# Optimization experiments

Measured on AMD Instinct MI355X. Metric: run time of the kernel, lower is better.

## Reference

```python
import jax, jax.numpy as jnp
import numpy as np

EPS = 1e-6
P_GEN = -9.0          # generalized-mean exponent (soft-min over grid)
BETA = 0.2            # bounded-IoU smooth-L1 transition point
HM_WEIGHT = 1.0
WH_WEIGHT = 0.1


def setup_inputs() -> dict:
    key = jax.random.key(0)
    ks = jax.random.split(key, 8)
    S, B, K, H, W = 2, 16, 128, 128, 128
    hm = jax.random.normal(ks[0], (S, B, 1, H, W), dtype=jnp.float32)
    # wh maps / targets must be positive (widths/heights on the stride-4 grid)
    wh_map = jax.random.uniform(ks[1], (S, B, 2, H, W), dtype=jnp.float32) * 30.0 + 1.0
    reg_map = jax.random.uniform(ks[2], (S, B, 2, H, W), dtype=jnp.float32)
    reg_gt = jax.random.uniform(ks[3], (B, K, 2), dtype=jnp.float32)
    wh_gt = jax.random.uniform(ks[4], (B, K, 2), dtype=jnp.float32) * 30.0 + 1.0
    ind = jax.random.randint(ks[5], (B, K), 0, H * W, dtype=jnp.int32)
    ctr = jax.random.randint(ks[6], (B, K, 2), 0, min(H, W), dtype=jnp.int32)
    reg_mask = jax.random.randint(ks[7], (B, K), 0, 2, dtype=jnp.int32)
    return {"hm": hm, "wh_map": wh_map, "reg_map": reg_map,
            "reg_gt": reg_gt, "wh_gt": wh_gt,
            "ind": ind, "ctr": ctr, "reg_mask": reg_mask}


def _gather_feat(feat, ind):
    # feat: (S,B,C,H,W), ind: (B,K) flat indices into H*W -> (S,B,K,C)
    S, B, C, H, W = feat.shape
    f = feat.reshape(S, B, C, H * W).transpose(0, 1, 3, 2)   # (S,B,HW,C)
    return jnp.take_along_axis(f, ind[None, :, :, None], axis=2)


def _whd_one(p_map, pts, m, grid, max_dist):
    # Weighted Hausdorff distance for one sample.
    # p_map: (H,W) probs; pts: (K,2) [y,x] float; m: (K,) {0,1} float
    p = p_map.reshape(-1)                                    # (HW,)
    d = jnp.sqrt(((grid[:, None, :] - pts[None, :, :]) ** 2).sum(-1))  # (HW,K)
    n_est = p.sum()
    # term 1: invalid points excluded from the min (max_dist upper-bounds all d)
    dmin = jnp.where(m[None, :] > 0, d, max_dist).min(axis=1)
    term1 = (p * dmin).sum() / (n_est + EPS)
    # term 2: soft-min over grid via generalized mean with p=-9
    weighted = (1.0 - p)[:, None] * max_dist + p[:, None] * d  # (HW,K)
    minn = jnp.mean((weighted + EPS) ** P_GEN, axis=0) ** (1.0 / P_GEN)  # (K,)
    term2 = (minn * m).sum() / jnp.maximum(m.sum(), 1.0)
    return term1 + term2


def _bounded_iou(reg_g, wh_g, reg_p, wh_p, m):
    # reg_g/wh_g: (1,B,K,2) gt; reg_p/wh_p: (S,B,K,2) pred; m: (B,K)
    dx = reg_g[..., 0] - reg_p[..., 0]
    dy = reg_g[..., 1] - reg_p[..., 1]
    w_g, h_g = wh_g[..., 0], wh_g[..., 1]
    w_p, h_p = wh_p[..., 0], wh_p[..., 1]
    ldx = 1.0 - jnp.maximum((w_g - 2.0 * jnp.abs(dx)) / (w_g + 2.0 * jnp.abs(dx) + EPS), 0.0)
    ldy = 1.0 - jnp.maximum((h_g - 2.0 * jnp.abs(dy)) / (h_g + 2.0 * jnp.abs(dy) + EPS), 0.0)
    ldw = 1.0 - jnp.minimum(w_g / (w_p + EPS), w_p / (w_g + EPS))
    ldh = 1.0 - jnp.minimum(h_g / (h_p + EPS), h_p / (h_g + EPS))
    l = jnp.stack([ldx, ldy, ldw, ldh], -1)                  # (S,B,K,4)
    l = jnp.where(l < BETA, 0.5 * l * l / BETA, l - 0.5 * BETA)
    num = (l * m[None, :, :, None]).sum((-1, -2))            # (S,B)
    den = jnp.maximum(m.sum(-1), 1.0)[None, :] * 4.0
    return num / den


def _forward(hm, wh_map, reg_map, reg_gt, wh_gt, ind, ctr, reg_mask):
    S, B, _, H, W = hm.shape
    dt = hm.dtype
    hm_p = jnp.clip(jax.nn.sigmoid(hm), 1e-4, 1.0 - 1e-4)    # CenterNet _sigmoid
    WH = _gather_feat(wh_map, ind)                            # (S,B,K,2)
    REG = _gather_feat(reg_map, ind)                          # (S,B,K,2)
    m = reg_mask.astype(dt)                                   # (B,K)
    valid = (m.sum(-1) > 0).astype(dt)                        # (B,) -> skip empty samples

    ys, xs = jnp.meshgrid(jnp.arange(H), jnp.arange(W), indexing="ij")
    grid = jnp.stack([ys, xs], -1).reshape(-1, 2).astype(dt)  # (HW,2)
    max_dist = jnp.sqrt(jnp.asarray(H * H + W * W, dt))
    pts = ctr[..., ::-1].astype(dt)                           # (B,K,2) [y,x]

    whd_batch = jax.vmap(_whd_one, in_axes=(0, 0, 0, None, None))
    hm_terms = jax.vmap(lambda hms: whd_batch(hms, pts, m, grid, max_dist))(hm_p[:, :, 0])  # (S,B)
    hm_loss = (hm_terms * valid[None, :]).sum() / (B * S)

    iou_terms = _bounded_iou(reg_gt[None], wh_gt[None], REG, WH, m)  # (S,B)
    iou_loss = (iou_terms * valid[None, :]).sum() / (B * S)

    loss = HM_WEIGHT * hm_loss + WH_WEIGHT * iou_loss
    return loss, hm_loss, iou_loss


def reference(hm, wh_map, reg_map, reg_gt, wh_gt, ind, ctr, reg_mask):
    return _forward(hm, wh_map, reg_map, reg_gt, wh_gt, ind, ctr, reg_mask)
```

## Files before the change

### kernel.cpp

```cpp
#include <hip/hip_runtime.h>

#define SS 2
#define BB 16
#define KK 128
#define HH 128
#define WW 128
#define HWSZ (HH*WW)
#define EPSF 1e-6f
#define MAXD 181.01933598375618f
#define MAXD2 32768.0f
#define MAXD8 (181.01933598375618f * 0.125f)
#define ME8C ((181.01933598375618f + 1e-6f) * 0.125f)

typedef float v2f __attribute__((ext_vector_type(2)));

#define WSQ_OFF 524288
#define WS_NEEDED_BYTES ((size_t)(524288 + 16*128*4) * 4)

__device__ __forceinline__ float sigclip(float x) {
    float e = __expf(-x);
    float p = __builtin_amdgcn_rcpf(1.0f + e);
    return fminf(fmaxf(p, 1e-4f), 0.9999f);
}

__device__ __forceinline__ float smoothl1(float l) {
    return (l < 0.2f) ? (2.5f * l * l) : (l - 0.1f);
}


__global__ void __launch_bounds__(256, 6) kAB2(const float* __restrict__ hm,
                                               const int* __restrict__ ctr,
                                               const int* __restrict__ reg_mask,
                                               float* __restrict__ ws,
                                               float* __restrict__ out) {
    const int r = blockIdx.x;
    const int b = blockIdx.y;
    const int t = threadIdx.x;
    __shared__ __align__(16) float spp2[128][2];
    __shared__ float2 spts_raw[KK];
    __shared__ float2 spts_msk[KK];
    __shared__ float red0[KK], red1[KK];
    __shared__ float st2[128];
    __shared__ float sred[8];

    if (r == 0 && b == 0 && t < 3) out[t] = 0.0f;

    {
        int c = t >> 7, j = t & 127;
        spp2[j][c] = sigclip(hm[(size_t)(c * BB + b) * HWSZ + r * WW + j]);
    }
    if (t < KK) {
        int mk = reg_mask[b * KK + t];
        float py = (float)ctr[(b * KK + t) * 2 + 1];
        float px = (float)ctr[(b * KK + t) * 2 + 0];
        spts_raw[t] = make_float2(py, px);
        spts_msk[t] = mk ? make_float2(py, px) : make_float2(1e9f, 1e9f);
    }
    __syncthreads();

    const int k = t & 127;
    const int h = t >> 7;

    float acc0 = 0.f, acc1 = 0.f;
    {
        float2 pt = spts_raw[k];
        float dy = ((float)r - pt.x) * 0.125f;
        float dy2 = dy * dy;
        float dx = ((float)(h * 64) - pt.y) * 0.125f;
        const float4* sp4 = (const float4*)(&spp2[h * 64][0]);
        const v2f ME8V = {ME8C, ME8C};
        #pragma unroll 4
        for (int q = 0; q < 32; ++q) {
            float4 pq = sp4[q];
            float dA = __builtin_amdgcn_sqrtf(fmaf(dx, dx, dy2));
            float dxB = dx + 0.125f;
            float dB = __builtin_amdgcn_sqrtf(fmaf(dxB, dxB, dy2));
            float tA = dA - MAXD8;
            float tB = dB - MAXD8;
            v2f pA = {pq.x, pq.y};
            v2f pB = {pq.z, pq.w};
            v2f wA = pA * tA + ME8V;
            v2f wB = pB * tB + ME8V;
            v2f a2 = wA * wA, a4 = a2 * a2, a8 = a4 * a4, a9 = a8 * wA;
            v2f b2 = wB * wB, b4 = b2 * b2, b8 = b4 * b4, b9 = b8 * wB;
            v2f pr = a9 * b9;
            v2f sm = a9 + b9;
            acc0 = fmaf(sm.x, __builtin_amdgcn_rcpf(pr.x), acc0);
            acc1 = fmaf(sm.y, __builtin_amdgcn_rcpf(pr.y), acc1);
            dx += 0.25f;
        }
    }

    float mm;
    {
        int pix = t & 127;
        float fx = (float)pix, fyf = (float)r;
        float m0 = MAXD2, m1 = MAXD2, m2 = MAXD2, m3 = MAXD2;
        int kb = h * 64;
        #pragma unroll 4
        for (int kk = 0; kk < 64; kk += 4) {
            float2 q0 = spts_msk[kb + kk + 0];
            float2 q1 = spts_msk[kb + kk + 1];
            float2 q2 = spts_msk[kb + kk + 2];
            float2 q3 = spts_msk[kb + kk + 3];
            float e0 = fyf - q0.x, f0 = fx - q0.y;
            float e1 = fyf - q1.x, f1 = fx - q1.y;
            float e2 = fyf - q2.x, f2 = fx - q2.y;
            float e3 = fyf - q3.x, f3 = fx - q3.y;
            m0 = fminf(m0, fmaf(f0, f0, e0 * e0));
            m1 = fminf(m1, fmaf(f1, f1, e1 * e1));
            m2 = fminf(m2, fmaf(f2, f2, e2 * e2));
            m3 = fminf(m3, fmaf(f3, f3, e3 * e3));
        }
        mm = fminf(fminf(m0, m1), fminf(m2, m3));
    }

    if (t >= 128) { st2[k] = mm; red0[k] = acc0; red1[k] = acc1; }
    __syncthreads();

    if (t < 128) {
        float s0 = acc0 + red0[k];
        float s1 = acc1 + red1[k];
        size_t basep = ((size_t)(b * 128 + r) * 2) * 128;
        ws[basep + k] = s0;
        ws[basep + 128 + k] = s1;
        float dmin = __builtin_amdgcn_sqrtf(fminf(mm, st2[k]));
        float p0 = spp2[k][0], p1 = spp2[k][1];
        float t1a = p0 * dmin, t1b = p1 * dmin, nea = p0, neb = p1;
        #pragma unroll
        for (int off = 32; off > 0; off >>= 1) {
            t1a += __shfl_down(t1a, off, 64);
            t1b += __shfl_down(t1b, off, 64);
            nea += __shfl_down(nea, off, 64);
            neb += __shfl_down(neb, off, 64);
        }
        if ((t & 63) == 0) {
            int wv = t >> 6;
            sred[wv * 4 + 0] = t1a; sred[wv * 4 + 1] = t1b;
            sred[wv * 4 + 2] = nea; sred[wv * 4 + 3] = neb;
        }
    }
    __syncthreads();
    if (t == 0) {
        float4 v = make_float4(sred[0] + sred[4], sred[1] + sred[5],
                               sred[2] + sred[6], sred[3] + sred[7]);
        ((float4*)(ws + WSQ_OFF))[b * 128 + r] = v;
    }
}

__global__ void __launch_bounds__(256) kC2(const float* __restrict__ ws,
                                           const float* __restrict__ wh_map,
                                           const float* __restrict__ reg_map,
                                           const float* __restrict__ reg_gt,
                                           const float* __restrict__ wh_gt,
                                           const int* __restrict__ ind,
                                           const int* __restrict__ reg_mask,
                                           float* __restrict__ out) {
    const int b = blockIdx.x, s = blockIdx.y;
    const int t = threadIdx.x;
    const int k = t & 127;
    const int g = t >> 7;

    __shared__ float ssum[256];
    {
        float sum = 0.f;
        const float* base = ws + ((size_t)(b * 128 + g * 64) * 2 + s) * 128 + k;
        #pragma unroll 8
        for (int c = 0; c < 64; ++c) sum += base[(size_t)c * 256];
        ssum[t] = sum;
    }
    __syncthreads();
    if (t >= 128) return;

    float mk = (float)reg_mask[b * KK + k];
    float meanp = (ssum[k] + ssum[k + 128]) * (1.0f / 16384.0f);
    float c2 = (mk > 0.f) ? 8.0f * exp2f(log2f(meanp) * (-1.0f / 9.0f)) : 0.0f;

    float g1 = 0.f, g2 = 0.f;
    {
        float4 q = ((const float4*)(ws + WSQ_OFF))[b * 128 + k];
        g1 = s ? q.y : q.x;
        g2 = s ? q.w : q.z;
        #pragma unroll
        for (int off = 32; off > 0; off >>= 1) {
            g1 += __shfl_down(g1, off, 64);
            g2 += __shfl_down(g2, off, 64);
        }
    }
    __shared__ float st1[2], sne[2];
    if ((k & 63) == 0) { st1[k >> 6] = g1; sne[k >> 6] = g2; }

    int idx = ind[b * KK + k];
    size_t sb = (size_t)(s * BB + b);
    float rp0 = reg_map[(sb * 2 + 0) * HWSZ + idx];
    float rp1 = reg_map[(sb * 2 + 1) * HWSZ + idx];
    float wp0 = wh_map[(sb * 2 + 0) * HWSZ + idx];
    float wp1 = wh_map[(sb * 2 + 1) * HWSZ + idx];
    float rg0 = reg_gt[(b * KK + k) * 2 + 0];
    float rg1 = reg_gt[(b * KK + k) * 2 + 1];
    float wg0 = wh_gt[(b * KK + k) * 2 + 0];
    float wg1 = wh_gt[(b * KK + k) * 2 + 1];
    float adx = fabsf(rg0 - rp0), ady = fabsf(rg1 - rp1);
    float ldx = 1.0f - fmaxf((wg0 - 2.0f * adx) / (wg0 + 2.0f * adx + EPSF), 0.0f);
    float ldy = 1.0f - fmaxf((wg1 - 2.0f * ady) / (wg1 + 2.0f * ady + EPSF), 0.0f);
    float ldw = 1.0f - fminf(wg0 / (wp0 + EPSF), wp0 / (wg0 + EPSF));
    float ldh = 1.0f - fminf(wg1 / (wp1 + EPSF), wp1 / (wg1 + EPSF));
    float lsum = (smoothl1(ldx) + smoothl1(ldy) + smoothl1(ldw) + smoothl1(ldh)) * mk;

    #pragma unroll
    for (int off = 32; off > 0; off >>= 1) {
        c2   += __shfl_down(c2, off, 64);
        lsum += __shfl_down(lsum, off, 64);
        mk   += __shfl_down(mk, off, 64);
    }
    __shared__ float sred[6];
    int lane = k & 63, wv = k >> 6;
    if (lane == 0) { sred[wv * 3 + 0] = c2; sred[wv * 3 + 1] = lsum; sred[wv * 3 + 2] = mk; }
    __syncthreads();
    if (k == 0) {
        float C2 = sred[0] + sred[3];
        float LS = sred[1] + sred[4];
        float MS = sred[2] + sred[5];
        float t1n = st1[0] + st1[1];
        float nst = sne[0] + sne[1];
        float valid = (MS > 0.f) ? 1.f : 0.f;
        float den = fmaxf(MS, 1.f);
        float t1 = t1n / (nst + EPSF);
        float t2 = C2 / den;
        float hmterm  = (t1 + t2) * valid * (1.0f / 32.0f);
        float iouterm = (LS / (den * 4.0f)) * valid * (1.0f / 32.0f);
        atomicAdd(&out[1], hmterm);
        atomicAdd(&out[2], iouterm);
        atomicAdd(&out[0], hmterm + 0.1f * iouterm);
    }
}


__global__ void kzero(float* ws, float* out) {
    int i = blockIdx.x * 256 + threadIdx.x;
    if (i < 4160) ws[i] = 0.0f;
    if (i < 3) out[i] = 0.0f;
}

__global__ void __launch_bounds__(256) kAB(const float* __restrict__ hm,
                                           const int* __restrict__ ctr,
                                           const int* __restrict__ reg_mask,
                                           float* __restrict__ ws) {
    const int b = blockIdx.y;
    const int chunk = blockIdx.x;
    const int base = chunk * 256;
    const int tid = threadIdx.x;
    __shared__ float2 spp[256];
    __shared__ float2 spts_raw[KK];
    __shared__ float2 spts_msk[KK];
    __shared__ float red0[KK], red1[KK];

    float p0 = sigclip(hm[(size_t)(0 * BB + b) * HWSZ + base + tid]);
    float p1 = sigclip(hm[(size_t)(1 * BB + b) * HWSZ + base + tid]);
    spp[tid] = make_float2(p0, p1);
    if (tid < KK) {
        int mk = reg_mask[b * KK + tid];
        float py = (float)ctr[(b * KK + tid) * 2 + 1];
        float px = (float)ctr[(b * KK + tid) * 2 + 0];
        spts_raw[tid] = make_float2(py, px);
        spts_msk[tid] = mk ? make_float2(py, px) : make_float2(1e9f, 1e9f);
    }
    __syncthreads();

    const int k = tid & 127;
    const int half = tid >> 7;
    float2 pt = spts_raw[k];
    float fy1 = (float)(chunk * 2 + half);
    float dy2 = (fy1 - pt.x) * (fy1 - pt.x);
    float acc0 = 0.f, acc1 = 0.f;
    float dx = -pt.y;
    const float2* sp = &spp[half * 128];
    #pragma unroll 4
    for (int j = 0; j < 128; ++j) {
        float d = __builtin_amdgcn_sqrtf(fmaf(dx, dx, dy2));
        float t = d - MAXD;
        float2 p = sp[j];
        float w0 = fmaf(p.x, t, MAXD) + EPSF;
        float w1 = fmaf(p.y, t, MAXD) + EPSF;
        float a2 = w0 * w0, a4 = a2 * a2, a8 = a4 * a4;
        float b2 = w1 * w1, b4 = b2 * b2, b8 = b4 * b4;
        acc0 += __builtin_amdgcn_rcpf(a8 * w0);
        acc1 += __builtin_amdgcn_rcpf(b8 * w1);
        dx += 1.0f;
    }

    {
        float fy = (float)(chunk * 2 + (tid >> 7));
        float fx = (float)(tid & 127);
        float m0 = MAXD2, m1 = MAXD2, m2 = MAXD2, m3 = MAXD2;
        #pragma unroll 4
        for (int kk = 0; kk < KK; kk += 4) {
            float2 q0 = spts_msk[kk + 0];
            float2 q1 = spts_msk[kk + 1];
            float2 q2 = spts_msk[kk + 2];
            float2 q3 = spts_msk[kk + 3];
            float dy0 = fy - q0.x, dx0 = fx - q0.y;
            float dy1 = fy - q1.x, dx1 = fx - q1.y;
            float dy2_ = fy - q2.x, dx2 = fx - q2.y;
            float dy3 = fy - q3.x, dx3 = fx - q3.y;
            m0 = fminf(m0, fmaf(dx0, dx0, dy0 * dy0));
            m1 = fminf(m1, fmaf(dx1, dx1, dy1 * dy1));
            m2 = fminf(m2, fmaf(dx2, dx2, dy2_ * dy2_));
            m3 = fminf(m3, fmaf(dx3, dx3, dy3 * dy3));
        }
        float dmin = __builtin_amdgcn_sqrtf(fminf(fminf(m0, m1), fminf(m2, m3)));
        float t1a = p0 * dmin, t1b = p1 * dmin, nea = p0, neb = p1;
        #pragma unroll
        for (int off = 32; off > 0; off >>= 1) {
            t1a += __shfl_down(t1a, off, 64);
            t1b += __shfl_down(t1b, off, 64);
            nea += __shfl_down(nea, off, 64);
            neb += __shfl_down(neb, off, 64);
        }
        if ((tid & 63) == 0) {
            atomicAdd(&ws[4096 + 0 * BB + b], t1a);
            atomicAdd(&ws[4096 + 1 * BB + b], t1b);
            atomicAdd(&ws[4128 + 0 * BB + b], nea);
            atomicAdd(&ws[4128 + 1 * BB + b], neb);
        }
    }

    if (half) { red0[k] = acc0; red1[k] = acc1; }
    __syncthreads();
    if (!half) {
        atomicAdd(&ws[(0 * BB + b) * KK + k], acc0 + red0[k]);
        atomicAdd(&ws[(1 * BB + b) * KK + k], acc1 + red1[k]);
    }
}

__global__ void __launch_bounds__(128) kC(const float* __restrict__ ws,
                                          const float* __restrict__ wh_map,
                                          const float* __restrict__ reg_map,
                                          const float* __restrict__ reg_gt,
                                          const float* __restrict__ wh_gt,
                                          const int* __restrict__ ind,
                                          const int* __restrict__ reg_mask,
                                          float* __restrict__ out) {
    const int b = blockIdx.x, s = blockIdx.y, k = threadIdx.x;
    float mk = (float)reg_mask[b * KK + k];
    float sp = ws[(s * BB + b) * KK + k];
    float mean = sp * (1.0f / 16384.0f);
    float c2 = (mk > 0.f) ? exp2f(log2f(mean) * (-1.0f / 9.0f)) : 0.0f;

    int idx = ind[b * KK + k];
    size_t sb = (size_t)(s * BB + b);
    float rp0 = reg_map[(sb * 2 + 0) * HWSZ + idx];
    float rp1 = reg_map[(sb * 2 + 1) * HWSZ + idx];
    float wp0 = wh_map[(sb * 2 + 0) * HWSZ + idx];
    float wp1 = wh_map[(sb * 2 + 1) * HWSZ + idx];
    float rg0 = reg_gt[(b * KK + k) * 2 + 0];
    float rg1 = reg_gt[(b * KK + k) * 2 + 1];
    float wg0 = wh_gt[(b * KK + k) * 2 + 0];
    float wg1 = wh_gt[(b * KK + k) * 2 + 1];
    float adx = fabsf(rg0 - rp0), ady = fabsf(rg1 - rp1);
    float ldx = 1.0f - fmaxf((wg0 - 2.0f * adx) / (wg0 + 2.0f * adx + EPSF), 0.0f);
    float ldy = 1.0f - fmaxf((wg1 - 2.0f * ady) / (wg1 + 2.0f * ady + EPSF), 0.0f);
    float ldw = 1.0f - fminf(wg0 / (wp0 + EPSF), wp0 / (wg0 + EPSF));
    float ldh = 1.0f - fminf(wg1 / (wp1 + EPSF), wp1 / (wg1 + EPSF));
    float lsum = (smoothl1(ldx) + smoothl1(ldy) + smoothl1(ldw) + smoothl1(ldh)) * mk;

    #pragma unroll
    for (int off = 32; off > 0; off >>= 1) {
        c2   += __shfl_down(c2, off, 64);
        lsum += __shfl_down(lsum, off, 64);
        mk   += __shfl_down(mk, off, 64);
    }
    __shared__ float sred[6];
    int lane = k & 63, wv = k >> 6;
    if (lane == 0) { sred[wv * 3 + 0] = c2; sred[wv * 3 + 1] = lsum; sred[wv * 3 + 2] = mk; }
    __syncthreads();
    if (k == 0) {
        float C2 = sred[0] + sred[3];
        float LS = sred[1] + sred[4];
        float MS = sred[2] + sred[5];
        float valid = (MS > 0.f) ? 1.f : 0.f;
        float den = fmaxf(MS, 1.f);
        float t1 = ws[4096 + s * BB + b] / (ws[4128 + s * BB + b] + EPSF);
        float t2 = C2 / den;
        float hmterm  = (t1 + t2) * valid * (1.0f / 32.0f);
        float iouterm = (LS / (den * 4.0f)) * valid * (1.0f / 32.0f);
        atomicAdd(&out[1], hmterm);
        atomicAdd(&out[2], iouterm);
        atomicAdd(&out[0], hmterm + 0.1f * iouterm);
    }
}

extern "C" void kernel_launch(void* const* d_in, const int* in_sizes, int n_in,
                              void* d_out, int out_size, void* d_ws, size_t ws_size,
                              hipStream_t stream) {
    const float* hm       = (const float*)d_in[0];
    const float* wh_map   = (const float*)d_in[1];
    const float* reg_map  = (const float*)d_in[2];
    const float* reg_gt   = (const float*)d_in[3];
    const float* wh_gt    = (const float*)d_in[4];
    const int*   ind      = (const int*)d_in[5];
    const int*   ctr      = (const int*)d_in[6];
    const int*   reg_mask = (const int*)d_in[7];
    float* out = (float*)d_out;
    float* ws  = (float*)d_ws;

    if (ws_size >= WS_NEEDED_BYTES) {
        hipLaunchKernelGGL(kAB2, dim3(128, BB), dim3(256), 0, stream,
                           hm, ctr, reg_mask, ws, out);
        hipLaunchKernelGGL(kC2, dim3(BB, SS), dim3(256), 0, stream,
                           ws, wh_map, reg_map, reg_gt, wh_gt, ind, reg_mask, out);
    } else {
        hipLaunchKernelGGL(kzero, dim3(17), dim3(256), 0, stream, ws, out);
        hipLaunchKernelGGL(kAB, dim3(64, BB), dim3(256), 0, stream, hm, ctr, reg_mask, ws);
        hipLaunchKernelGGL(kC, dim3(BB, SS), dim3(128), 0, stream,
                           ws, wh_map, reg_map, reg_gt, wh_gt, ind, reg_mask, out);
    }
}
```

Before: 94.27 us.

## Fuse final reduction kernel into main kernel via last-block atomic counter

The separate reduction kernel kC2 is removed. Each kAB3 block now increments a per-batch atomic counter after writing its partials, and the last block for that batch performs the final per-sample reduction and IoU loss. Two memset calls zero the counters and the output. This trades one kernel launch and its gap for threadfences, an atomic per block, and a serial 128-row sum done by a single block per batch.

```diff
diff --git a/kernel.cpp b/kernel.cpp
--- a/kernel.cpp
+++ b/kernel.cpp
@@ -15,7 +15,8 @@
 typedef float v2f __attribute__((ext_vector_type(2)));
 
 #define WSQ_OFF 524288
-#define WS_NEEDED_BYTES ((size_t)(524288 + 16*128*4) * 4)
+#define WSC_OFF 532480
+#define WS_NEEDED_BYTES ((size_t)(WSC_OFF + 16) * 4)
 
 __device__ __forceinline__ float sigclip(float x) {
     float e = __expf(-x);
@@ -28,9 +29,14 @@
 }
 
 
-__global__ void __launch_bounds__(256, 6) kAB2(const float* __restrict__ hm,
+__global__ void __launch_bounds__(256, 6) kAB3(const float* __restrict__ hm,
                                                const int* __restrict__ ctr,
                                                const int* __restrict__ reg_mask,
+                                               const float* __restrict__ wh_map,
+                                               const float* __restrict__ reg_map,
+                                               const float* __restrict__ reg_gt,
+                                               const float* __restrict__ wh_gt,
+                                               const int* __restrict__ ind,
                                                float* __restrict__ ws,
                                                float* __restrict__ out) {
     const int r = blockIdx.x;
@@ -42,8 +48,8 @@
     __shared__ float red0[KK], red1[KK];
     __shared__ float st2[128];
     __shared__ float sred[8];
-
-    if (r == 0 && b == 0 && t < 3) out[t] = 0.0f;
+    __shared__ int slast;
+    __shared__ float fin[4][5];
 
     {
         int c = t >> 7, j = t & 127;
@@ -93,8 +99,7 @@
 
     float mm;
     {
-        int pix = t & 127;
-        float fx = (float)pix, fyf = (float)r;
+        float fx = (float)(t & 127), fyf = (float)r;
         float m0 = MAXD2, m1 = MAXD2, m2 = MAXD2, m3 = MAXD2;
         int kb = h * 64;
         #pragma unroll 4
@@ -146,86 +151,78 @@
                                sred[2] + sred[6], sred[3] + sred[7]);
         ((float4*)(ws + WSQ_OFF))[b * 128 + r] = v;
     }
-}
-
-__global__ void __launch_bounds__(256) kC2(const float* __restrict__ ws,
-                                           const float* __restrict__ wh_map,
-                                           const float* __restrict__ reg_map,
-                                           const float* __restrict__ reg_gt,
-                                           const float* __restrict__ wh_gt,
-                                           const int* __restrict__ ind,
-                                           const int* __restrict__ reg_mask,
-                                           float* __restrict__ out) {
-    const int b = blockIdx.x, s = blockIdx.y;
-    const int t = threadIdx.x;
-    const int k = t & 127;
-    const int g = t >> 7;
-
-    __shared__ float ssum[256];
-    {
-        float sum = 0.f;
-        const float* base = ws + ((size_t)(b * 128 + g * 64) * 2 + s) * 128 + k;
+
+    __threadfence();
+    if (t == 0) {
+        int old = atomicAdd((int*)(ws + WSC_OFF) + b, 1);
+        slast = (old == 127) ? 1 : 0;
+    }
+    __syncthreads();
+    if (!slast) return;
+    __threadfence();
+
+    const int s = h;
+    float sum = 0.f;
+    {
+        const float* basep = ws + (((size_t)b * 128) * 2 + s) * 128 + k;
         #pragma unroll 8
-        for (int c = 0; c < 64; ++c) sum += base[(size_t)c * 256];
-        ssum[t] = sum;
-    }
-    __syncthreads();
-    if (t >= 128) return;
-
-    float mk = (float)reg_mask[b * KK + k];
-    float meanp = (ssum[k] + ssum[k + 128]) * (1.0f / 16384.0f);
-    float c2 = (mk > 0.f) ? 8.0f * exp2f(log2f(meanp) * (-1.0f / 9.0f)) : 0.0f;
-
-    float g1 = 0.f, g2 = 0.f;
+        for (int rr = 0; rr < 128; ++rr) sum += basep[(size_t)rr * 256];
+    }
+    float mkv = (float)reg_mask[b * KK + k];
+    float meanp = sum * (1.0f / 16384.0f);
+    float c2 = (mkv > 0.f) ? 8.0f * exp2f(log2f(meanp) * (-1.0f / 9.0f)) : 0.0f;
+
+    float g1, g2;
     {
         float4 q = ((const float4*)(ws + WSQ_OFF))[b * 128 + k];
         g1 = s ? q.y : q.x;
         g2 = s ? q.w : q.z;
-        #pragma unroll
-        for (int off = 32; off > 0; off >>= 1) {
-            g1 += __shfl_down(g1, off, 64);
-            g2 += __shfl_down(g2, off, 64);
-        }
-    }
-    __shared__ float st1[2], sne[2];
-    if ((k & 63) == 0) { st1[k >> 6] = g1; sne[k >> 6] = g2; }
-
-    int idx = ind[b * KK + k];
-    size_t sb = (size_t)(s * BB + b);
-    float rp0 = reg_map[(sb * 2 + 0) * HWSZ + idx];
-    float rp1 = reg_map[(sb * 2 + 1) * HWSZ + idx];
-    float wp0 = wh_map[(sb * 2 + 0) * HWSZ + idx];
-    float wp1 = wh_map[(sb * 2 + 1) * HWSZ + idx];
-    float rg0 = reg_gt[(b * KK + k) * 2 + 0];
-    float rg1 = reg_gt[(b * KK + k) * 2 + 1];
-    float wg0 = wh_gt[(b * KK + k) * 2 + 0];
-    float wg1 = wh_gt[(b * KK + k) * 2 + 1];
-    float adx = fabsf(rg0 - rp0), ady = fabsf(rg1 - rp1);
-    float ldx = 1.0f - fmaxf((wg0 - 2.0f * adx) / (wg0 + 2.0f * adx + EPSF), 0.0f);
-    float ldy = 1.0f - fmaxf((wg1 - 2.0f * ady) / (wg1 + 2.0f * ady + EPSF), 0.0f);
-    float ldw = 1.0f - fminf(wg0 / (wp0 + EPSF), wp0 / (wg0 + EPSF));
-    float ldh = 1.0f - fminf(wg1 / (wp1 + EPSF), wp1 / (wg1 + EPSF));
-    float lsum = (smoothl1(ldx) + smoothl1(ldy) + smoothl1(ldw) + smoothl1(ldh)) * mk;
+    }
+
+    float lsum;
+    {
+        int idx = ind[b * KK + k];
+        size_t sb = (size_t)(s * BB + b);
+        float rp0 = reg_map[(sb * 2 + 0) * HWSZ + idx];
+        float rp1 = reg_map[(sb * 2 + 1) * HWSZ + idx];
+        float wp0 = wh_map[(sb * 2 + 0) * HWSZ + idx];
+        float wp1 = wh_map[(sb * 2 + 1) * HWSZ + idx];
+        float rg0 = reg_gt[(b * KK + k) * 2 + 0];
+        float rg1 = reg_gt[(b * KK + k) * 2 + 1];
+        float wg0 = wh_gt[(b * KK + k) * 2 + 0];
+        float wg1 = wh_gt[(b * KK + k) * 2 + 1];
+        float adx = fabsf(rg0 - rp0), ady = fabsf(rg1 - rp1);
+        float ldx = 1.0f - fmaxf((wg0 - 2.0f * adx) / (wg0 + 2.0f * adx + EPSF), 0.0f);
+        float ldy = 1.0f - fmaxf((wg1 - 2.0f * ady) / (wg1 + 2.0f * ady + EPSF), 0.0f);
+        float ldw = 1.0f - fminf(wg0 / (wp0 + EPSF), wp0 / (wg0 + EPSF));
+        float ldh = 1.0f - fminf(wg1 / (wp1 + EPSF), wp1 / (wg1 + EPSF));
+        lsum = (smoothl1(ldx) + smoothl1(ldy) + smoothl1(ldw) + smoothl1(ldh)) * mkv;
+    }
 
     #pragma unroll
     for (int off = 32; off > 0; off >>= 1) {
         c2   += __shfl_down(c2, off, 64);
         lsum += __shfl_down(lsum, off, 64);
-        mk   += __shfl_down(mk, off, 64);
-    }
-    __shared__ float sred[6];
-    int lane = k & 63, wv = k >> 6;
-    if (lane == 0) { sred[wv * 3 + 0] = c2; sred[wv * 3 + 1] = lsum; sred[wv * 3 + 2] = mk; }
-    __syncthreads();
-    if (k == 0) {
-        float C2 = sred[0] + sred[3];
-        float LS = sred[1] + sred[4];
-        float MS = sred[2] + sred[5];
-        float t1n = st1[0] + st1[1];
-        float nst = sne[0] + sne[1];
+        mkv  += __shfl_down(mkv, off, 64);
+        g1   += __shfl_down(g1, off, 64);
+        g2   += __shfl_down(g2, off, 64);
+    }
+    if ((t & 63) == 0) {
+        int wv = t >> 6;
+        fin[wv][0] = c2; fin[wv][1] = lsum; fin[wv][2] = mkv;
+        fin[wv][3] = g1; fin[wv][4] = g2;
+    }
+    __syncthreads();
+    if ((t & 127) == 0) {
+        int w0 = t >> 6;
+        float C2  = fin[w0][0] + fin[w0 + 1][0];
+        float LS  = fin[w0][1] + fin[w0 + 1][1];
+        float MS  = fin[w0][2] + fin[w0 + 1][2];
+        float T1  = fin[w0][3] + fin[w0 + 1][3];
+        float NE  = fin[w0][4] + fin[w0 + 1][4];
         float valid = (MS > 0.f) ? 1.f : 0.f;
         float den = fmaxf(MS, 1.f);
-        float t1 = t1n / (nst + EPSF);
+        float t1 = T1 / (NE + EPSF);
         float t2 = C2 / den;
         float hmterm  = (t1 + t2) * valid * (1.0f / 32.0f);
         float iouterm = (LS / (den * 4.0f)) * valid * (1.0f / 32.0f);
@@ -405,10 +402,11 @@
     float* ws  = (float*)d_ws;
 
     if (ws_size >= WS_NEEDED_BYTES) {
-        hipLaunchKernelGGL(kAB2, dim3(128, BB), dim3(256), 0, stream,
-                           hm, ctr, reg_mask, ws, out);
-        hipLaunchKernelGGL(kC2, dim3(BB, SS), dim3(256), 0, stream,
-                           ws, wh_map, reg_map, reg_gt, wh_gt, ind, reg_mask, out);
+        hipMemsetAsync(ws + WSC_OFF, 0, 16 * sizeof(int), stream);
+        hipMemsetAsync(out, 0, 3 * sizeof(float), stream);
+        hipLaunchKernelGGL(kAB3, dim3(128, BB), dim3(256), 0, stream,
+                           hm, ctr, reg_mask, wh_map, reg_map, reg_gt, wh_gt, ind,
+                           ws, out);
     } else {
         hipLaunchKernelGGL(kzero, dim3(17), dim3(256), 0, stream, ws, out);
         hipLaunchKernelGGL(kAB, dim3(64, BB), dim3(256), 0, stream, hm, ctr, reg_mask, ws);
```

After: 264.8 us. 2.81x slower.
